# Performance work log

Measured on AMD Instinct MI355X. Metric: run time of the kernel, lower is better.

## Reference

```python
import jax, jax.numpy as jnp
import numpy as np

B, D, H, G, WR = 8192, 1024, 1024, 2, 64
URANKS = [64, 64]


def setup_inputs() -> dict:
    key = jax.random.key(0)
    ks = jax.random.split(key, 12)
    s = 0.1
    return {
        "x": jax.random.normal(ks[0], (B, D), jnp.float32),
        "h": jax.random.normal(ks[1], (B, H), jnp.float32),
        "c": jax.random.normal(ks[2], (B, H), jnp.float32),
        "dia_x": s * jax.random.normal(ks[3], (1, D), jnp.float32),
        "dia_h": s * jax.random.normal(ks[4], (1, H), jnp.float32),
        "Ux": s * jax.random.normal(ks[5], (D, WR), jnp.float32),
        "Vx": s * jax.random.normal(ks[6], (4 * H, WR), jnp.float32),
        "Uh_0": s * jax.random.normal(ks[7], (G, H // G, URANKS[0]), jnp.float32),
        "Vh_0": s * jax.random.normal(ks[8], (G, URANKS[0], 4 * (H // G)), jnp.float32),
        "Uh_1": s * jax.random.normal(ks[9], (G, H // G, URANKS[1]), jnp.float32),
        "Vh_1": s * jax.random.normal(ks[10], (G, URANKS[1], 4 * (H // G)), jnp.float32),
        "bias_x": jnp.ones((1, 4 * H), jnp.float32),
        "bias_h": jnp.ones((1, 4 * H), jnp.float32),
    }


def reference(x, h, c, dia_x, dia_h, Ux, Vx, Uh_0, Vh_0, Uh_1, Vh_1, bias_x, bias_h):
    Bn, Dn = x.shape
    Hn = h.shape[1]
    g = Uh_0.shape[0]
    Hg = Hn // g
    r0 = Uh_0.shape[2]

    # diagonal (vector-multiplication) paths, x-part zero-padded to hidden width
    vm_x = jnp.pad(dia_x * x, ((0, 0), (0, Hn - Dn)))          # [B, H]
    vm_h = dia_h * h                                           # [B, H]

    # low-rank input projection
    lowered_x = (x @ Ux) @ Vx.T                                # [B, 4H]

    # refined diagonal corrections subtracted from the low-rank outputs
    Vx4 = Vx.reshape(4, Hn, -1)[:, :Dn, :]                     # [4, D, wR]
    coef_x = jnp.sum(Ux[None, :, :] * Vx4, axis=-1)            # [4, D]
    vm_refined_x = jnp.pad(x[:, None, :] * coef_x[None], ((0, 0), (0, 0), (0, Hn - Dn))).reshape(Bn, 4 * Hn)

    Uh0f = Uh_0.reshape(Hn, r0)                                # [H, r0]
    Vh0f = jnp.transpose(Vh_0, (0, 2, 1)).reshape(4 * Hn, r0).reshape(4, Hn, r0)
    coef_h = jnp.sum(Uh0f[None, :, :] * Vh0f, axis=-1)         # [4, H]
    vm_refined_h = (h[:, None, :] * coef_h[None]).reshape(Bn, 4 * Hn)

    gx = lowered_x - vm_refined_x + bias_x
    xi, xf, xo, xn = jnp.split(gx, 4, axis=1)

    # grouped low-rank recurrent projection with cyclic group permutation
    hv = h.reshape(Bn, g, Hg)
    Uhs = [Uh_0, Uh_1]
    Vhs = [Vh_0, Vh_1]
    g_h = jnp.zeros((Bn, 4 * Hn), x.dtype)
    for i in range(g):
        idx = np.roll(np.arange(g), -i)                        # static permutation
        hp = hv[:, idx, :]                                     # [B, g, H/g]
        t = jnp.einsum('bgn,gnr->bgr', hp, Uhs[i])             # [B, g, r_i]
        t = jnp.einsum('bgr,grm->bgm', t, Vhs[i])              # [B, g, 4H/g]
        g_h = g_h + t.reshape(Bn, 4 * Hn)

    gh = g_h - vm_refined_h + bias_h
    hf, hi, hn, ho = jnp.split(gh, 4, axis=1)                  # note gate order differs from x

    base = vm_x + vm_h
    inputgate = jax.nn.sigmoid(xi + hi + base)
    forgetgate = jax.nn.sigmoid(xf + hf + base)
    outputgate = jax.nn.sigmoid(xo + ho + base)
    newgate = jnp.tanh(xn + hn + base)

    c_next = forgetgate * c + inputgate * newgate
    h_next = outputgate * jnp.tanh(c_next)
    return (h_next, c_next)
```

## Files before the change

kernel.cpp:

```cpp
#include <hip/hip_runtime.h>


typedef _Float16 half8 __attribute__((ext_vector_type(8)));
typedef _Float16 half4v __attribute__((ext_vector_type(4)));
typedef float f32x4 __attribute__((ext_vector_type(4)));

#define WS_U1F   0
#define WS_UH1F  131072
#define WS_W2    393216
#define WS_CX    1966080
#define WS_CH    1982464
#define WS_BB    1998848

__global__ __launch_bounds__(256) void prep_kernel(
    const float* __restrict__ Ux, const float* __restrict__ Vx,
    const float* __restrict__ Uh0, const float* __restrict__ Vh0,
    const float* __restrict__ Uh1, const float* __restrict__ Vh1,
    const float* __restrict__ dia_x, const float* __restrict__ dia_h,
    const float* __restrict__ bias_x, const float* __restrict__ bias_h,
    _Float16* __restrict__ U1f, _Float16* __restrict__ Uh1f,
    _Float16* __restrict__ W2f, float* __restrict__ cx,
    float* __restrict__ ch, float* __restrict__ bb)
{
    __shared__ __align__(16) _Float16 Tl[64][260];

    const int tid = threadIdx.x;
    if (blockIdx.x >= 240) {
        int bid2 = blockIdx.x - 240;
        int s = bid2 & 1, i = (bid2 >> 1) & 1, mchunk = bid2 >> 2;
        const float* Vh = i ? Vh1 : Vh0;
        #pragma unroll
        for (int it = 0; it < 16; ++it) {
            int idx = tid + it * 256;
            int row = idx >> 6, c4 = idx & 63;
            f32x4 v = *(const f32x4*)&Vh[(size_t)(s * 64 + row) * 2048
                                         + mchunk * 256 + c4 * 4];
            half4v p;
            p[0] = (_Float16)v[0]; p[1] = (_Float16)v[1];
            p[2] = (_Float16)v[2]; p[3] = (_Float16)v[3];
            *(half4v*)&Tl[row][c4 * 4] = p;
        }
        __syncthreads();
        int lane = tid & 63, l15 = lane & 15, quad = lane >> 4;
        #pragma unroll
        for (int q = 0; q < 8; ++q) {
            int combo = (tid >> 6) * 8 + q;
            int ct_local = combo >> 1, rk = combo & 1;
            int m_local = ct_local * 16 + l15;
            int m = mchunk * 256 + m_local;
            int g01 = (m >= 1024) ? 0 : 1;
            int ct_global = (m - (1 - g01) * 1024) >> 4;
            int ksq = 2 + 2 * i + rk;
            half8 v8;
            #pragma unroll
            for (int jj = 0; jj < 8; ++jj)
                v8[jj] = Tl[rk * 32 + quad * 8 + jj][m_local];
            size_t t_out = (((size_t)(s * 2 + g01) * 64 + ct_global) * 6 + ksq) * 64 + lane;
            *(half8*)&W2f[t_out * 8] = v8;
        }
        return;
    }

    int e = blockIdx.x * 256 + tid;
    if (e < 8192) {
        int lane = e & 63, ks = (e >> 6) & 31, ct = e >> 11;
        int l15 = lane & 15, quad = lane >> 4;
        half8 v8;
        #pragma unroll
        for (int jj = 0; jj < 8; ++jj) {
            int k = ks * 32 + quad * 8 + jj;
            v8[jj] = (_Float16)Ux[k * 64 + ct * 16 + l15];
        }
        *(half8*)&U1f[(size_t)e * 8] = v8;
    } else if (e < 24576) {
        int t = e - 8192;
        int lane = t & 63, ks = (t >> 6) & 15, ct = (t >> 10) & 3, j = t >> 12;
        int l15 = lane & 15, quad = lane >> 4;
        const float* src = (j & 1) ? Uh1 : Uh0;
        int g = j >> 1;
        half8 v8;
        #pragma unroll
        for (int jj = 0; jj < 8; ++jj) {
            int k = ks * 32 + quad * 8 + jj;
            v8[jj] = (_Float16)src[(g * 512 + k) * 64 + ct * 16 + l15];
        }
        *(half8*)&Uh1f[(size_t)t * 8] = v8;
    } else if (e < 57344) {
        int tt = e - 24576;
        int lane = tt & 63;
        int ksq2 = (tt >> 6) & 1;
        int ct   = (tt / 128) & 63;
        int g01  = (tt / 8192) & 1;
        int s    = tt / 16384;
        int l15 = lane & 15, quad = lane >> 4;
        int k = ct * 16 + l15;
        int jx = s * 2 + g01;
        half8 v8;
        #pragma unroll
        for (int jj = 0; jj < 8; ++jj) {
            int r = ksq2 * 32 + quad * 8 + jj;
            v8[jj] = (_Float16)Vx[(jx * 1024 + k) * 64 + r];
        }
        size_t t_out = (((size_t)(s * 2 + g01) * 64 + ct) * 6 + ksq2) * 64 + lane;
        *(half8*)&W2f[t_out * 8] = v8;
    } else if (e < 61440) {
        int t = e - 57344;
        int q = t >> 10; int k = t & 1023;
        int jh = q ^ 1;
        int fh = jh * 1024 + k; int g = fh >> 11; int m = fh & 2047;
        float sx0 = 0.f, sx1 = 0.f, sh0 = 0.f, sh1 = 0.f;
        #pragma unroll 4
        for (int r = 0; r < 64; r += 2) {
            sx0 += Ux[k * 64 + r]     * Vx[(q * 1024 + k) * 64 + r];
            sx1 += Ux[k * 64 + r + 1] * Vx[(q * 1024 + k) * 64 + r + 1];
            sh0 += Uh0[k * 64 + r]     * Vh0[(size_t)(g * 64 + r) * 2048 + m];
            sh1 += Uh0[k * 64 + r + 1] * Vh0[(size_t)(g * 64 + r + 1) * 2048 + m];
        }
        cx[t] = dia_x[k] - (sx0 + sx1);
        ch[t] = dia_h[k] - (sh0 + sh1);
        bb[t] = bias_x[q * 1024 + k] + bias_h[jh * 1024 + k];
    }
}

__global__ __launch_bounds__(1024) void fused_kernel(
    const float* __restrict__ x, const float* __restrict__ h,
    const float* __restrict__ c,
    const _Float16* __restrict__ U1f, const _Float16* __restrict__ Uh1f,
    const _Float16* __restrict__ W2f,
    const float* __restrict__ cx, const float* __restrict__ ch,
    const float* __restrict__ bb, float* __restrict__ out)
{
    __shared__ __align__(16) _Float16 Xsh[32][1032];
    __shared__ __align__(16) _Float16 Hsh[32][1032];
    __shared__ __align__(16) _Float16 Tsh[32][328];

    const int tid = threadIdx.x;
    const int w = tid >> 6, l = tid & 63, l15 = l & 15, quad = l >> 4;
    const int b0 = blockIdx.x * 32;
    const size_t rowbase = (size_t)b0 * 1024;

    {
        const float* xs = x + rowbase;
        const float* hs = h + rowbase;
        #pragma unroll
        for (int ii = 0; ii < 8; ++ii) {
            int idx = tid + ii * 1024;
            int row = idx >> 8, c4 = idx & 255;
            f32x4 fx = __builtin_nontemporal_load(
                (const f32x4*)&xs[(size_t)row * 1024 + c4 * 4]);
            f32x4 fh = __builtin_nontemporal_load(
                (const f32x4*)&hs[(size_t)row * 1024 + c4 * 4]);
            half4v px, ph;
            px[0] = (_Float16)fx[0]; px[1] = (_Float16)fx[1];
            px[2] = (_Float16)fx[2]; px[3] = (_Float16)fx[3];
            ph[0] = (_Float16)fh[0]; ph[1] = (_Float16)fh[1];
            ph[2] = (_Float16)fh[2]; ph[3] = (_Float16)fh[3];
            *(half4v*)&Xsh[row][c4 * 4] = px;
            *(half4v*)&Hsh[row][c4 * 4] = ph;
        }
    }
    __syncthreads();

    if (w < 8) {
        int rt = w & 1, ct = w >> 1;
        f32x4 acc = {};
        const _Float16* bp = U1f + ((size_t)(ct * 32) * 64 + l) * 8;
        #pragma unroll
        for (int ks = 0; ks < 32; ++ks) {
            half8 a = *(const half8*)&Xsh[rt * 16 + l15][ks * 32 + quad * 8];
            half8 b = *(const half8*)(bp + (size_t)ks * 512);
            acc = __builtin_amdgcn_mfma_f32_16x16x32_f16(a, b, acc, 0, 0, 0);
        }
        #pragma unroll
        for (int r = 0; r < 4; ++r)
            Tsh[rt * 16 + quad * 4 + r][ct * 16 + l15] = (_Float16)acc[r];
    }
    {
        int pstart = (w < 8) ? w : 8 + (w - 8) * 3;
        int pcnt   = (w < 8) ? 1 : 3;
        for (int ii = 0; ii < 3; ++ii) {
            if (ii >= pcnt) break;
            int p = pstart + ii;
            int j = p >> 3, rem = p & 7, prt = rem >> 2, pct = rem & 3;
            int hoff = (j == 1 || j == 2) ? 512 : 0;
            f32x4 pa = {};
            const _Float16* pb = Uh1f + ((size_t)((j * 4 + pct) * 16) * 64 + l) * 8;
            #pragma unroll
            for (int ks = 0; ks < 16; ++ks) {
                half8 a = *(const half8*)&Hsh[prt * 16 + l15][hoff + ks * 32 + quad * 8];
                half8 b = *(const half8*)(pb + (size_t)ks * 512);
                pa = __builtin_amdgcn_mfma_f32_16x16x32_f16(a, b, pa, 0, 0, 0);
            }
            #pragma unroll
            for (int r = 0; r < 4; ++r)
                Tsh[prt * 16 + quad * 4 + r][64 + j * 64 + pct * 16 + l15] = (_Float16)pa[r];
        }
    }
    __syncthreads();

    const int secIF[3] = {0, 64, 128};
    const int secON[3] = {0, 192, 256};

    float cpref[2][2][4];
    {
        int k0 = w * 16 + l15;
        #pragma unroll
        for (int rt = 0; rt < 2; ++rt)
            #pragma unroll
            for (int r = 0; r < 4; ++r)
                cpref[0][rt][r] = __builtin_nontemporal_load(
                    &c[rowbase + (size_t)(rt * 16 + quad * 4 + r) * 1024 + k0]);
    }

    #pragma unroll
    for (int i = 0; i < 4; ++i) {
        const int ctg = w + 16 * i;
        const int k = ctg * 16 + l15;

        if (i < 3) {
            int kn = k + 256;
            #pragma unroll
            for (int rt = 0; rt < 2; ++rt)
                #pragma unroll
                for (int r = 0; r < 4; ++r)
                    cpref[(i + 1) & 1][rt][r] = __builtin_nontemporal_load(
                        &c[rowbase + (size_t)(rt * 16 + quad * 4 + r) * 1024 + kn]);
        }

        float cxi = cx[k], cxf = cx[1024 + k], cxo = cx[2048 + k], cxn = cx[3072 + k];
        float chi = ch[k], chf = ch[1024 + k], cho = ch[2048 + k], chn = ch[3072 + k];
        float bbi = bb[k], bbf = bb[1024 + k], bbo = bb[2048 + k], bbn = bb[3072 + k];

        const size_t laneoff = (size_t)l * 8;
        const _Float16* bpi = W2f + (size_t)((0 * 64 + ctg) * 6) * 512 + laneoff;
        const _Float16* bpf = W2f + (size_t)((1 * 64 + ctg) * 6) * 512 + laneoff;
        const _Float16* bpo = W2f + (size_t)((2 * 64 + ctg) * 6) * 512 + laneoff;
        const _Float16* bpn = W2f + (size_t)((3 * 64 + ctg) * 6) * 512 + laneoff;

        f32x4 acc[4][2] = {};
        #pragma unroll
        for (int ks = 0; ks < 6; ++ks) {
            half8 bi = *(const half8*)(bpi + (size_t)ks * 512);
            half8 bf = *(const half8*)(bpf + (size_t)ks * 512);
            half8 bo = *(const half8*)(bpo + (size_t)ks * 512);
            half8 bn = *(const half8*)(bpn + (size_t)ks * 512);
            int coff = (ks & 1) * 32 + quad * 8;
            #pragma unroll
            for (int rt = 0; rt < 2; ++rt) {
                half8 aA = *(const half8*)&Tsh[rt * 16 + l15][secIF[ks >> 1] + coff];
                half8 aB = *(const half8*)&Tsh[rt * 16 + l15][secON[ks >> 1] + coff];
                acc[0][rt] = __builtin_amdgcn_mfma_f32_16x16x32_f16(aA, bi, acc[0][rt], 0, 0, 0);
                acc[1][rt] = __builtin_amdgcn_mfma_f32_16x16x32_f16(aA, bf, acc[1][rt], 0, 0, 0);
                acc[2][rt] = __builtin_amdgcn_mfma_f32_16x16x32_f16(aB, bo, acc[2][rt], 0, 0, 0);
                acc[3][rt] = __builtin_amdgcn_mfma_f32_16x16x32_f16(aB, bn, acc[3][rt], 0, 0, 0);
            }
        }

        #pragma unroll
        for (int rt = 0; rt < 2; ++rt) {
            #pragma unroll
            for (int r = 0; r < 4; ++r) {
                int rl = rt * 16 + quad * 4 + r;
                size_t off = rowbase + (size_t)rl * 1024 + k;
                float xv = (float)Xsh[rl][k];
                float hv = (float)Hsh[rl][k];
                float cvv = cpref[i & 1][rt][r];
                float pi = acc[0][rt][r] + xv * cxi + hv * chi + bbi;
                float pf = acc[1][rt][r] + xv * cxf + hv * chf + bbf;
                float po = acc[2][rt][r] + xv * cxo + hv * cho + bbo;
                float pn = acc[3][rt][r] + xv * cxn + hv * chn + bbn;
                float ig = __builtin_amdgcn_rcpf(1.f + __expf(-pi));
                float fg = __builtin_amdgcn_rcpf(1.f + __expf(-pf));
                float og = __builtin_amdgcn_rcpf(1.f + __expf(-po));
                float ng = 1.f - 2.f * __builtin_amdgcn_rcpf(__expf(2.f * pn) + 1.f);
                float cn = fg * cvv + ig * ng;
                float tc = 1.f - 2.f * __builtin_amdgcn_rcpf(__expf(2.f * cn) + 1.f);
                out[off] = og * tc;
                out[(size_t)8388608 + off] = cn;
            }
        }
    }
}

extern "C" void kernel_launch(void* const* d_in, const int* in_sizes, int n_in,
                              void* d_out, int out_size, void* d_ws, size_t ws_size,
                              hipStream_t stream)
{
    const float* x      = (const float*)d_in[0];
    const float* h      = (const float*)d_in[1];
    const float* c      = (const float*)d_in[2];
    const float* dia_x  = (const float*)d_in[3];
    const float* dia_h  = (const float*)d_in[4];
    const float* Ux     = (const float*)d_in[5];
    const float* Vx     = (const float*)d_in[6];
    const float* Uh0    = (const float*)d_in[7];
    const float* Vh0    = (const float*)d_in[8];
    const float* Uh1    = (const float*)d_in[9];
    const float* Vh1    = (const float*)d_in[10];
    const float* bias_x = (const float*)d_in[11];
    const float* bias_h = (const float*)d_in[12];
    float* out = (float*)d_out;

    char* ws = (char*)d_ws;
    _Float16* U1f  = (_Float16*)(ws + WS_U1F);
    _Float16* Uh1f = (_Float16*)(ws + WS_UH1F);
    _Float16* W2f  = (_Float16*)(ws + WS_W2);
    float* cx = (float*)(ws + WS_CX);
    float* ch = (float*)(ws + WS_CH);
    float* bb = (float*)(ws + WS_BB);

    prep_kernel<<<272, 256, 0, stream>>>(Ux, Vx, Uh0, Vh0, Uh1, Vh1,
                                         dia_x, dia_h, bias_x, bias_h,
                                         U1f, Uh1f, W2f, cx, ch, bb);
    fused_kernel<<<256, 1024, 0, stream>>>(x, h, c, U1f, Uh1f, W2f,
                                           cx, ch, bb, out);
}
```

Measured before the change: 208.0 us.

## Double-buffer W2 fragment loads and prefetch gate corrections in fused kernel epilogue GEMM

Restructures the second-stage MFMA loop into a software pipeline. The W2 B-fragments for the next k-step, and for the next column tile, are loaded while the current step's MFMAs issue. The cx/ch/bb correction vectors are now prefetched one iteration ahead, MFMA blocks are wrapped in s_setprio, and launch bounds request 4 waves per SIMD. Nontemporal loads of x, h and c are replaced with ordinary loads. These changes aim to hide global-load latency behind matrix work, at the cost of more registers, which the occupancy hint may turn into spills.

```diff
diff --git a/kernel.cpp b/kernel.cpp
--- a/kernel.cpp
+++ b/kernel.cpp
@@ -122,7 +122,35 @@
     }
 }
 
-__global__ __launch_bounds__(1024) void fused_kernel(
+#define LOADB(B_, ct_, ks_)                                                    \
+    {                                                                          \
+        const size_t _o = (size_t)(ks_) * 512 + laneoff;                       \
+        B_[0] = *(const half8*)(W2f + (size_t)((0 * 64 + (ct_)) * 6) * 512 + _o); \
+        B_[1] = *(const half8*)(W2f + (size_t)((1 * 64 + (ct_)) * 6) * 512 + _o); \
+        B_[2] = *(const half8*)(W2f + (size_t)((2 * 64 + (ct_)) * 6) * 512 + _o); \
+        B_[3] = *(const half8*)(W2f + (size_t)((3 * 64 + (ct_)) * 6) * 512 + _o); \
+    }
+
+#define DOMFMA(B_, ks_)                                                        \
+    {                                                                          \
+        const int _co = ((ks_) & 1) * 32 + quad * 8;                           \
+        half8 aA0 = *(const half8*)&Tsh[l15][secIF[(ks_) >> 1] + _co];         \
+        half8 aB0 = *(const half8*)&Tsh[l15][secON[(ks_) >> 1] + _co];         \
+        half8 aA1 = *(const half8*)&Tsh[16 + l15][secIF[(ks_) >> 1] + _co];    \
+        half8 aB1 = *(const half8*)&Tsh[16 + l15][secON[(ks_) >> 1] + _co];    \
+        __builtin_amdgcn_s_setprio(1);                                         \
+        acc[0][0] = __builtin_amdgcn_mfma_f32_16x16x32_f16(aA0, B_[0], acc[0][0], 0, 0, 0); \
+        acc[1][0] = __builtin_amdgcn_mfma_f32_16x16x32_f16(aA0, B_[1], acc[1][0], 0, 0, 0); \
+        acc[2][0] = __builtin_amdgcn_mfma_f32_16x16x32_f16(aB0, B_[2], acc[2][0], 0, 0, 0); \
+        acc[3][0] = __builtin_amdgcn_mfma_f32_16x16x32_f16(aB0, B_[3], acc[3][0], 0, 0, 0); \
+        acc[0][1] = __builtin_amdgcn_mfma_f32_16x16x32_f16(aA1, B_[0], acc[0][1], 0, 0, 0); \
+        acc[1][1] = __builtin_amdgcn_mfma_f32_16x16x32_f16(aA1, B_[1], acc[1][1], 0, 0, 0); \
+        acc[2][1] = __builtin_amdgcn_mfma_f32_16x16x32_f16(aB1, B_[2], acc[2][1], 0, 0, 0); \
+        acc[3][1] = __builtin_amdgcn_mfma_f32_16x16x32_f16(aB1, B_[3], acc[3][1], 0, 0, 0); \
+        __builtin_amdgcn_s_setprio(0);                                         \
+    }
+
+__global__ __launch_bounds__(1024, 4) void fused_kernel(
     const float* __restrict__ x, const float* __restrict__ h,
     const float* __restrict__ c,
     const _Float16* __restrict__ U1f, const _Float16* __restrict__ Uh1f,
@@ -146,10 +174,8 @@
         for (int ii = 0; ii < 8; ++ii) {
             int idx = tid + ii * 1024;
             int row = idx >> 8, c4 = idx & 255;
-            f32x4 fx = __builtin_nontemporal_load(
-                (const f32x4*)&xs[(size_t)row * 1024 + c4 * 4]);
-            f32x4 fh = __builtin_nontemporal_load(
-                (const f32x4*)&hs[(size_t)row * 1024 + c4 * 4]);
+            f32x4 fx = *(const f32x4*)&xs[(size_t)row * 1024 + c4 * 4];
+            f32x4 fh = *(const f32x4*)&hs[(size_t)row * 1024 + c4 * 4];
             half4v px, ph;
             px[0] = (_Float16)fx[0]; px[1] = (_Float16)fx[1];
             px[2] = (_Float16)fx[2]; px[3] = (_Float16)fx[3];
@@ -198,63 +224,59 @@
     }
     __syncthreads();
 
-    const int secIF[3] = {0, 64, 128};
-    const int secON[3] = {0, 192, 256};
-
+    constexpr int secIF[3] = {0, 64, 128};
+    constexpr int secON[3] = {0, 192, 256};
+    const size_t laneoff = (size_t)l * 8;
+
+    half8 bA[4], bB[4];
+    float corrC[12], corrN[12];
     float cpref[2][2][4];
+
     {
-        int k0 = w * 16 + l15;
+        const int k0 = w * 16 + l15;
+        #pragma unroll
+        for (int q = 0; q < 4; ++q) {
+            corrC[q]     = cx[q * 1024 + k0];
+            corrC[4 + q] = ch[q * 1024 + k0];
+            corrC[8 + q] = bb[q * 1024 + k0];
+        }
         #pragma unroll
         for (int rt = 0; rt < 2; ++rt)
             #pragma unroll
             for (int r = 0; r < 4; ++r)
-                cpref[0][rt][r] = __builtin_nontemporal_load(
-                    &c[rowbase + (size_t)(rt * 16 + quad * 4 + r) * 1024 + k0]);
+                cpref[0][rt][r] = c[rowbase + (size_t)(rt * 16 + quad * 4 + r) * 1024 + k0];
+        LOADB(bA, w, 0);
     }
 
     #pragma unroll
     for (int i = 0; i < 4; ++i) {
         const int ctg = w + 16 * i;
         const int k = ctg * 16 + l15;
+        f32x4 acc[4][2] = {};
+
+        LOADB(bB, ctg, 1);  DOMFMA(bA, 0);
+        LOADB(bA, ctg, 2);  DOMFMA(bB, 1);
+        LOADB(bB, ctg, 3);  DOMFMA(bA, 2);
+        LOADB(bA, ctg, 4);  DOMFMA(bB, 3);
+        LOADB(bB, ctg, 5);  DOMFMA(bA, 4);
 
         if (i < 3) {
-            int kn = k + 256;
+            const int kn = k + 256;
+            LOADB(bA, ctg + 16, 0);
             #pragma unroll
             for (int rt = 0; rt < 2; ++rt)
                 #pragma unroll
                 for (int r = 0; r < 4; ++r)
-                    cpref[(i + 1) & 1][rt][r] = __builtin_nontemporal_load(
-                        &c[rowbase + (size_t)(rt * 16 + quad * 4 + r) * 1024 + kn]);
-        }
-
-        float cxi = cx[k], cxf = cx[1024 + k], cxo = cx[2048 + k], cxn = cx[3072 + k];
-        float chi = ch[k], chf = ch[1024 + k], cho = ch[2048 + k], chn = ch[3072 + k];
-        float bbi = bb[k], bbf = bb[1024 + k], bbo = bb[2048 + k], bbn = bb[3072 + k];
-
-        const size_t laneoff = (size_t)l * 8;
-        const _Float16* bpi = W2f + (size_t)((0 * 64 + ctg) * 6) * 512 + laneoff;
-        const _Float16* bpf = W2f + (size_t)((1 * 64 + ctg) * 6) * 512 + laneoff;
-        const _Float16* bpo = W2f + (size_t)((2 * 64 + ctg) * 6) * 512 + laneoff;
-        const _Float16* bpn = W2f + (size_t)((3 * 64 + ctg) * 6) * 512 + laneoff;
-
-        f32x4 acc[4][2] = {};
-        #pragma unroll
-        for (int ks = 0; ks < 6; ++ks) {
-            half8 bi = *(const half8*)(bpi + (size_t)ks * 512);
-            half8 bf = *(const half8*)(bpf + (size_t)ks * 512);
-            half8 bo = *(const half8*)(bpo + (size_t)ks * 512);
-            half8 bn = *(const half8*)(bpn + (size_t)ks * 512);
-            int coff = (ks & 1) * 32 + quad * 8;
-            #pragma unroll
-            for (int rt = 0; rt < 2; ++rt) {
-                half8 aA = *(const half8*)&Tsh[rt * 16 + l15][secIF[ks >> 1] + coff];
-                half8 aB = *(const half8*)&Tsh[rt * 16 + l15][secON[ks >> 1] + coff];
-                acc[0][rt] = __builtin_amdgcn_mfma_f32_16x16x32_f16(aA, bi, acc[0][rt], 0, 0, 0);
-                acc[1][rt] = __builtin_amdgcn_mfma_f32_16x16x32_f16(aA, bf, acc[1][rt], 0, 0, 0);
-                acc[2][rt] = __builtin_amdgcn_mfma_f32_16x16x32_f16(aB, bo, acc[2][rt], 0, 0, 0);
-                acc[3][rt] = __builtin_amdgcn_mfma_f32_16x16x32_f16(aB, bn, acc[3][rt], 0, 0, 0);
+                    cpref[(i + 1) & 1][rt][r] =
+                        c[rowbase + (size_t)(rt * 16 + quad * 4 + r) * 1024 + kn];
+            #pragma unroll
+            for (int q = 0; q < 4; ++q) {
+                corrN[q]     = cx[q * 1024 + kn];
+                corrN[4 + q] = ch[q * 1024 + kn];
+                corrN[8 + q] = bb[q * 1024 + kn];
             }
         }
+        DOMFMA(bB, 5);
 
         #pragma unroll
         for (int rt = 0; rt < 2; ++rt) {
@@ -265,10 +287,10 @@
                 float xv = (float)Xsh[rl][k];
                 float hv = (float)Hsh[rl][k];
                 float cvv = cpref[i & 1][rt][r];
-                float pi = acc[0][rt][r] + xv * cxi + hv * chi + bbi;
-                float pf = acc[1][rt][r] + xv * cxf + hv * chf + bbf;
-                float po = acc[2][rt][r] + xv * cxo + hv * cho + bbo;
-                float pn = acc[3][rt][r] + xv * cxn + hv * chn + bbn;
+                float pi = acc[0][rt][r] + xv * corrC[0] + hv * corrC[4] + corrC[8];
+                float pf = acc[1][rt][r] + xv * corrC[1] + hv * corrC[5] + corrC[9];
+                float po = acc[2][rt][r] + xv * corrC[2] + hv * corrC[6] + corrC[10];
+                float pn = acc[3][rt][r] + xv * corrC[3] + hv * corrC[7] + corrC[11];
                 float ig = __builtin_amdgcn_rcpf(1.f + __expf(-pi));
                 float fg = __builtin_amdgcn_rcpf(1.f + __expf(-pf));
                 float og = __builtin_amdgcn_rcpf(1.f + __expf(-po));
@@ -279,6 +301,8 @@
                 out[(size_t)8388608 + off] = cn;
             }
         }
+        #pragma unroll
+        for (int q = 0; q < 12; ++q) corrC[q] = corrN[q];
     }
 }
 
```

After: 333.4 us. 1.6x slower.

## Shrink fused block to 16 rows and read x/h directly from global

Applied to the files above, without the earlier changes.

The fused kernel now handles 16 rows per block with 512 threads across 512 blocks, instead of 32 rows with 1024 threads across 256 blocks. The big fp16 shared-memory staging of x and h is removed: MFMA A-operands are converted from global fp32 on the fly, and the epilogue reloads x, h and c from global memory. The c software prefetch is also dropped. This frees LDS and may allow more blocks per CU, at the cost of reading x and h from global twice and losing the prefetch latency hiding.

```diff
diff --git a/kernel.cpp b/kernel.cpp
--- a/kernel.cpp
+++ b/kernel.cpp
@@ -122,7 +122,19 @@
     }
 }
 
-__global__ __launch_bounds__(1024) void fused_kernel(
+static __device__ __forceinline__ half8 cvt8(const float* p)
+{
+    f32x4 u = *(const f32x4*)p;
+    f32x4 v = *(const f32x4*)(p + 4);
+    half8 a;
+    a[0] = (_Float16)u[0]; a[1] = (_Float16)u[1];
+    a[2] = (_Float16)u[2]; a[3] = (_Float16)u[3];
+    a[4] = (_Float16)v[0]; a[5] = (_Float16)v[1];
+    a[6] = (_Float16)v[2]; a[7] = (_Float16)v[3];
+    return a;
+}
+
+__global__ __launch_bounds__(512) void fused_kernel(
     const float* __restrict__ x, const float* __restrict__ h,
     const float* __restrict__ c,
     const _Float16* __restrict__ U1f, const _Float16* __restrict__ Uh1f,
@@ -130,114 +142,71 @@
     const float* __restrict__ cx, const float* __restrict__ ch,
     const float* __restrict__ bb, float* __restrict__ out)
 {
-    __shared__ __align__(16) _Float16 Xsh[32][1032];
-    __shared__ __align__(16) _Float16 Hsh[32][1032];
-    __shared__ __align__(16) _Float16 Tsh[32][328];
+    __shared__ __align__(16) _Float16 Tsh[16][328];
 
     const int tid = threadIdx.x;
     const int w = tid >> 6, l = tid & 63, l15 = l & 15, quad = l >> 4;
-    const int b0 = blockIdx.x * 32;
+    const int b0 = blockIdx.x * 16;
     const size_t rowbase = (size_t)b0 * 1024;
 
-    {
-        const float* xs = x + rowbase;
-        const float* hs = h + rowbase;
-        #pragma unroll
-        for (int ii = 0; ii < 8; ++ii) {
-            int idx = tid + ii * 1024;
-            int row = idx >> 8, c4 = idx & 255;
-            f32x4 fx = __builtin_nontemporal_load(
-                (const f32x4*)&xs[(size_t)row * 1024 + c4 * 4]);
-            f32x4 fh = __builtin_nontemporal_load(
-                (const f32x4*)&hs[(size_t)row * 1024 + c4 * 4]);
-            half4v px, ph;
-            px[0] = (_Float16)fx[0]; px[1] = (_Float16)fx[1];
-            px[2] = (_Float16)fx[2]; px[3] = (_Float16)fx[3];
-            ph[0] = (_Float16)fh[0]; ph[1] = (_Float16)fh[1];
-            ph[2] = (_Float16)fh[2]; ph[3] = (_Float16)fh[3];
-            *(half4v*)&Xsh[row][c4 * 4] = px;
-            *(half4v*)&Hsh[row][c4 * 4] = ph;
-        }
-    }
-    __syncthreads();
-
-    if (w < 8) {
-        int rt = w & 1, ct = w >> 1;
+    if (w < 4) {
+        int ct = w;
         f32x4 acc = {};
+        const float* xrow = x + (size_t)(b0 + l15) * 1024 + quad * 8;
         const _Float16* bp = U1f + ((size_t)(ct * 32) * 64 + l) * 8;
         #pragma unroll
         for (int ks = 0; ks < 32; ++ks) {
-            half8 a = *(const half8*)&Xsh[rt * 16 + l15][ks * 32 + quad * 8];
+            half8 a = cvt8(xrow + ks * 32);
             half8 b = *(const half8*)(bp + (size_t)ks * 512);
             acc = __builtin_amdgcn_mfma_f32_16x16x32_f16(a, b, acc, 0, 0, 0);
         }
         #pragma unroll
         for (int r = 0; r < 4; ++r)
-            Tsh[rt * 16 + quad * 4 + r][ct * 16 + l15] = (_Float16)acc[r];
+            Tsh[quad * 4 + r][ct * 16 + l15] = (_Float16)acc[r];
     }
     {
-        int pstart = (w < 8) ? w : 8 + (w - 8) * 3;
-        int pcnt   = (w < 8) ? 1 : 3;
+        int pstart = (w < 4) ? w : 4 + (w - 4) * 3;
+        int pcnt   = (w < 4) ? 1 : 3;
         for (int ii = 0; ii < 3; ++ii) {
             if (ii >= pcnt) break;
             int p = pstart + ii;
-            int j = p >> 3, rem = p & 7, prt = rem >> 2, pct = rem & 3;
+            int j = p >> 2, pct = p & 3;
             int hoff = (j == 1 || j == 2) ? 512 : 0;
             f32x4 pa = {};
+            const float* hrow = h + (size_t)(b0 + l15) * 1024 + hoff + quad * 8;
             const _Float16* pb = Uh1f + ((size_t)((j * 4 + pct) * 16) * 64 + l) * 8;
             #pragma unroll
             for (int ks = 0; ks < 16; ++ks) {
-                half8 a = *(const half8*)&Hsh[prt * 16 + l15][hoff + ks * 32 + quad * 8];
+                half8 a = cvt8(hrow + ks * 32);
                 half8 b = *(const half8*)(pb + (size_t)ks * 512);
                 pa = __builtin_amdgcn_mfma_f32_16x16x32_f16(a, b, pa, 0, 0, 0);
             }
             #pragma unroll
             for (int r = 0; r < 4; ++r)
-                Tsh[prt * 16 + quad * 4 + r][64 + j * 64 + pct * 16 + l15] = (_Float16)pa[r];
+                Tsh[quad * 4 + r][64 + j * 64 + pct * 16 + l15] = (_Float16)pa[r];
         }
     }
     __syncthreads();
 
     const int secIF[3] = {0, 64, 128};
     const int secON[3] = {0, 192, 256};
-
-    float cpref[2][2][4];
-    {
-        int k0 = w * 16 + l15;
-        #pragma unroll
-        for (int rt = 0; rt < 2; ++rt)
-            #pragma unroll
-            for (int r = 0; r < 4; ++r)
-                cpref[0][rt][r] = __builtin_nontemporal_load(
-                    &c[rowbase + (size_t)(rt * 16 + quad * 4 + r) * 1024 + k0]);
-    }
+    const size_t laneoff = (size_t)l * 8;
 
     #pragma unroll
-    for (int i = 0; i < 4; ++i) {
-        const int ctg = w + 16 * i;
+    for (int i = 0; i < 8; ++i) {
+        const int ctg = w + 8 * i;
         const int k = ctg * 16 + l15;
-
-        if (i < 3) {
-            int kn = k + 256;
-            #pragma unroll
-            for (int rt = 0; rt < 2; ++rt)
-                #pragma unroll
-                for (int r = 0; r < 4; ++r)
-                    cpref[(i + 1) & 1][rt][r] = __builtin_nontemporal_load(
-                        &c[rowbase + (size_t)(rt * 16 + quad * 4 + r) * 1024 + kn]);
-        }
 
         float cxi = cx[k], cxf = cx[1024 + k], cxo = cx[2048 + k], cxn = cx[3072 + k];
         float chi = ch[k], chf = ch[1024 + k], cho = ch[2048 + k], chn = ch[3072 + k];
         float bbi = bb[k], bbf = bb[1024 + k], bbo = bb[2048 + k], bbn = bb[3072 + k];
 
-        const size_t laneoff = (size_t)l * 8;
         const _Float16* bpi = W2f + (size_t)((0 * 64 + ctg) * 6) * 512 + laneoff;
         const _Float16* bpf = W2f + (size_t)((1 * 64 + ctg) * 6) * 512 + laneoff;
         const _Float16* bpo = W2f + (size_t)((2 * 64 + ctg) * 6) * 512 + laneoff;
         const _Float16* bpn = W2f + (size_t)((3 * 64 + ctg) * 6) * 512 + laneoff;
 
-        f32x4 acc[4][2] = {};
+        f32x4 acc[4] = {};
         #pragma unroll
         for (int ks = 0; ks < 6; ++ks) {
             half8 bi = *(const half8*)(bpi + (size_t)ks * 512);
@@ -245,39 +214,33 @@
             half8 bo = *(const half8*)(bpo + (size_t)ks * 512);
             half8 bn = *(const half8*)(bpn + (size_t)ks * 512);
             int coff = (ks & 1) * 32 + quad * 8;
-            #pragma unroll
-            for (int rt = 0; rt < 2; ++rt) {
-                half8 aA = *(const half8*)&Tsh[rt * 16 + l15][secIF[ks >> 1] + coff];
-                half8 aB = *(const half8*)&Tsh[rt * 16 + l15][secON[ks >> 1] + coff];
-                acc[0][rt] = __builtin_amdgcn_mfma_f32_16x16x32_f16(aA, bi, acc[0][rt], 0, 0, 0);
-                acc[1][rt] = __builtin_amdgcn_mfma_f32_16x16x32_f16(aA, bf, acc[1][rt], 0, 0, 0);
-                acc[2][rt] = __builtin_amdgcn_mfma_f32_16x16x32_f16(aB, bo, acc[2][rt], 0, 0, 0);
-                acc[3][rt] = __builtin_amdgcn_mfma_f32_16x16x32_f16(aB, bn, acc[3][rt], 0, 0, 0);
-            }
-        }
-
-        #pragma unroll
-        for (int rt = 0; rt < 2; ++rt) {
-            #pragma unroll
-            for (int r = 0; r < 4; ++r) {
-                int rl = rt * 16 + quad * 4 + r;
-                size_t off = rowbase + (size_t)rl * 1024 + k;
-                float xv = (float)Xsh[rl][k];
-                float hv = (float)Hsh[rl][k];
-                float cvv = cpref[i & 1][rt][r];
-                float pi = acc[0][rt][r] + xv * cxi + hv * chi + bbi;
-                float pf = acc[1][rt][r] + xv * cxf + hv * chf + bbf;
-                float po = acc[2][rt][r] + xv * cxo + hv * cho + bbo;
-                float pn = acc[3][rt][r] + xv * cxn + hv * chn + bbn;
-                float ig = __builtin_amdgcn_rcpf(1.f + __expf(-pi));
-                float fg = __builtin_amdgcn_rcpf(1.f + __expf(-pf));
-                float og = __builtin_amdgcn_rcpf(1.f + __expf(-po));
-                float ng = 1.f - 2.f * __builtin_amdgcn_rcpf(__expf(2.f * pn) + 1.f);
-                float cn = fg * cvv + ig * ng;
-                float tc = 1.f - 2.f * __builtin_amdgcn_rcpf(__expf(2.f * cn) + 1.f);
-                out[off] = og * tc;
-                out[(size_t)8388608 + off] = cn;
-            }
+            half8 aA = *(const half8*)&Tsh[l15][secIF[ks >> 1] + coff];
+            half8 aB = *(const half8*)&Tsh[l15][secON[ks >> 1] + coff];
+            acc[0] = __builtin_amdgcn_mfma_f32_16x16x32_f16(aA, bi, acc[0], 0, 0, 0);
+            acc[1] = __builtin_amdgcn_mfma_f32_16x16x32_f16(aA, bf, acc[1], 0, 0, 0);
+            acc[2] = __builtin_amdgcn_mfma_f32_16x16x32_f16(aB, bo, acc[2], 0, 0, 0);
+            acc[3] = __builtin_amdgcn_mfma_f32_16x16x32_f16(aB, bn, acc[3], 0, 0, 0);
+        }
+
+        #pragma unroll
+        for (int r = 0; r < 4; ++r) {
+            int rl = quad * 4 + r;
+            size_t off = rowbase + (size_t)rl * 1024 + k;
+            float xv = x[off];
+            float hv = h[off];
+            float cvv = c[off];
+            float pi = acc[0][r] + xv * cxi + hv * chi + bbi;
+            float pf = acc[1][r] + xv * cxf + hv * chf + bbf;
+            float po = acc[2][r] + xv * cxo + hv * cho + bbo;
+            float pn = acc[3][r] + xv * cxn + hv * chn + bbn;
+            float ig = __builtin_amdgcn_rcpf(1.f + __expf(-pi));
+            float fg = __builtin_amdgcn_rcpf(1.f + __expf(-pf));
+            float og = __builtin_amdgcn_rcpf(1.f + __expf(-po));
+            float ng = 1.f - 2.f * __builtin_amdgcn_rcpf(__expf(2.f * pn) + 1.f);
+            float cn = fg * cvv + ig * ng;
+            float tc = 1.f - 2.f * __builtin_amdgcn_rcpf(__expf(2.f * cn) + 1.f);
+            out[off] = og * tc;
+            out[(size_t)8388608 + off] = cn;
         }
     }
 }
@@ -312,6 +275,6 @@
     prep_kernel<<<272, 256, 0, stream>>>(Ux, Vx, Uh0, Vh0, Uh1, Vh1,
                                          dia_x, dia_h, bias_x, bias_h,
                                          U1f, Uh1f, W2f, cx, ch, bb);
-    fused_kernel<<<256, 1024, 0, stream>>>(x, h, c, U1f, Uh1f, W2f,
-                                           cx, ch, bb, out);
-}
+    fused_kernel<<<512, 512, 0, stream>>>(x, h, c, U1f, Uh1f, W2f,
+                                          cx, ch, bb, out);
+}
```

After: 267.0 us. +28.4%, slower.
